# Optimization experiments

Measured on AMD Instinct MI355X. Metric: run time of the kernel, lower is better.

The kernel has to match this reference:

```python
import jax, jax.numpy as jnp
import numpy as np

BLOCK = 64      # block_size
NRAND = 3       # num_random_blocks
NUM_HEAD = 16
HEAD_DIM = 64
HIDDEN = 1024
PEN = -10000.0  # HF attn_mask_penalty


def _sparse_attn(q, k, v, band_mask, from_mask, to_mask, blocked_mask, rand_attn):
    # q,k,v: [B,H,S,D]; BigBird block-sparse attention (HF math).
    B, H, S, D = q.shape
    b, r = BLOCK, NRAND
    n = S // b
    rsd = 1.0 / (D ** 0.5)

    bq = q.reshape(B, H, n, b, D)
    bk = k.reshape(B, H, n, b, D)
    bv = v.reshape(B, H, n, b, D)

    bi = jnp.arange(B)[:, None, None, None]
    hi = jnp.arange(H)[None, :, None, None]
    # gathered random key/value blocks: [B,H,n-2,r*b,D]
    gk = bk[bi, hi, rand_attn].reshape(B, H, n - 2, r * b, D)
    gv = bv[bi, hi, rand_attn].reshape(B, H, n - 2, r * b, D)
    # random-block mask: [B,H,n-2,b,r*b]
    rm = blocked_mask[bi, rand_attn].reshape(B, H, n - 2, r * b)
    rand_mask = jnp.einsum("blq,bhlk->bhlqk", blocked_mask[:, 1:-1], rm)

    ones = lambda shp: jnp.ones(shp, q.dtype)

    # ---- first query block: attends to everything ----
    p = jnp.einsum("bhqd,bhkd->bhqk", bq[:, :, 0], k) * rsd + (1.0 - to_mask) * PEN
    c0 = jnp.einsum("bhqk,bhkd->bhqd", jax.nn.softmax(p, -1), v)[:, :, None]

    # ---- second query block: blocks 0,1,2,last + random ----
    k1 = jnp.concatenate([bk[:, :, 0], bk[:, :, 1], bk[:, :, 2], bk[:, :, -1], gk[:, :, 0]], axis=2)
    v1 = jnp.concatenate([bv[:, :, 0], bv[:, :, 1], bv[:, :, 2], bv[:, :, -1], gv[:, :, 0]], axis=2)
    p = jnp.einsum("bhqd,bhkd->bhqk", bq[:, :, 1], k1) * rsd
    seq_pad = jnp.concatenate([to_mask[..., :3 * b], to_mask[..., -b:], ones((B, 1, 1, r * b))], axis=3)
    rand_pad = jnp.concatenate([ones((B, H, b, 4 * b)), rand_mask[:, :, 0]], axis=3)
    p = p + (1.0 - jnp.minimum(seq_pad, rand_pad)) * PEN
    c1 = jnp.einsum("bhqk,bhkd->bhqd", jax.nn.softmax(p, -1), v1)[:, :, None]

    # ---- middle blocks 2..n-3: band(3 blocks) + first + last + random ----
    ek = jnp.concatenate([bk[:, :, 1:-3], bk[:, :, 2:-2], bk[:, :, 3:-1]], axis=3)  # [B,H,n-4,3b,D]
    ev = jnp.concatenate([bv[:, :, 1:-3], bv[:, :, 2:-2], bv[:, :, 3:-1]], axis=3)
    mq = bq[:, :, 2:-2]                                                              # [B,H,n-4,b,D]
    inner = jnp.einsum("bhlqd,bhlkd->bhlqk", mq, ek) * rsd + (1.0 - band_mask) * PEN
    randp = jnp.einsum("bhlqd,bhlkd->bhlqk", mq, gk[:, :, 1:-1]) * rsd + (1.0 - rand_mask[:, :, 1:-1]) * PEN
    firstp = jnp.einsum("bhlqd,bhkd->bhlqk", mq, bk[:, :, 0]) * rsd + (1.0 - to_mask[..., :b][:, :, None]) * PEN
    lastp = jnp.einsum("bhlqd,bhkd->bhlqk", mq, bk[:, :, -1]) * rsd + (1.0 - to_mask[..., -b:][:, :, None]) * PEN
    band = jnp.concatenate([firstp, inner, randp, lastp], axis=-1)  # [B,H,n-4,b,(5+r)*b]
    a = jax.nn.softmax(band, -1)
    cm = jnp.einsum("bhlqk,bhlkd->bhlqd", a[..., b:4 * b], ev)
    cm = cm + jnp.einsum("bhlqk,bhlkd->bhlqd", a[..., 4 * b:-b], gv[:, :, 1:-1])
    cm = cm + jnp.einsum("bhlqk,bhkd->bhlqd", a[..., :b], bv[:, :, 0])
    cm = cm + jnp.einsum("bhlqk,bhkd->bhlqd", a[..., -b:], bv[:, :, -1])

    # ---- second-last query block: blocks 0,-3,-2,-1 + random ----
    k2 = jnp.concatenate([bk[:, :, 0], bk[:, :, -3], bk[:, :, -2], bk[:, :, -1], gk[:, :, -1]], axis=2)
    v2 = jnp.concatenate([bv[:, :, 0], bv[:, :, -3], bv[:, :, -2], bv[:, :, -1], gv[:, :, -1]], axis=2)
    p = jnp.einsum("bhqd,bhkd->bhqk", bq[:, :, -2], k2) * rsd
    seq_pad = jnp.concatenate([to_mask[..., :b], to_mask[..., -3 * b:], ones((B, 1, 1, r * b))], axis=3)
    rand_pad = jnp.concatenate([ones((B, H, b, 4 * b)), rand_mask[:, :, -1]], axis=3)
    p = p + (1.0 - jnp.minimum(seq_pad, rand_pad)) * PEN
    c2 = jnp.einsum("bhqk,bhkd->bhqd", jax.nn.softmax(p, -1), v2)[:, :, None]

    # ---- last query block: attends to everything ----
    p = jnp.einsum("bhqd,bhkd->bhqk", bq[:, :, -1], k) * rsd + (1.0 - to_mask) * PEN
    c3 = jnp.einsum("bhqk,bhkd->bhqd", jax.nn.softmax(p, -1), v)[:, :, None]

    ctx = jnp.concatenate([c0, c1, cm, c2, c3], axis=2).reshape(B, H, S, D)
    ctx = ctx * from_mask  # [B,1,S,1]
    return ctx.transpose(0, 2, 1, 3).reshape(B, S, H * D)


def setup_inputs() -> dict:
    key = jax.random.key(0)
    ks = jax.random.split(key, 12)
    B, L = 2, 4064
    S = 4096
    n = S // BLOCK
    sc = 0.02
    inp = {
        "X": jax.random.normal(ks[0], (B, L, HIDDEN), jnp.float32),
        "Wq": jax.random.normal(ks[1], (HIDDEN, NUM_HEAD * HEAD_DIM), jnp.float32) * sc,
        "b_q": jnp.zeros((NUM_HEAD * HEAD_DIM,), jnp.float32),
        "Wk": jax.random.normal(ks[2], (HIDDEN, NUM_HEAD * HEAD_DIM), jnp.float32) * sc,
        "b_k": jnp.zeros((NUM_HEAD * HEAD_DIM,), jnp.float32),
        "Wv": jax.random.normal(ks[3], (HIDDEN, NUM_HEAD * HEAD_DIM), jnp.float32) * sc,
        "b_v": jnp.zeros((NUM_HEAD * HEAD_DIM,), jnp.float32),
        "Wo": jax.random.normal(ks[4], (NUM_HEAD * HEAD_DIM, HIDDEN), jnp.float32) * sc,
        "b_o": jnp.zeros((HIDDEN,), jnp.float32),
        "band_mask": jnp.ones((B, 1, n - 4, BLOCK, 3 * BLOCK), jnp.float32),
        "from_mask": jnp.ones((B, 1, S, 1), jnp.float32),
        "to_mask": jnp.ones((B, 1, 1, S), jnp.float32),
        "blocked_encoder_mask": jnp.ones((B, n, BLOCK), jnp.float32),
        "rand_attn": jax.random.randint(ks[5], (B, NUM_HEAD, n - 2, NRAND), 0, n, jnp.int32),
    }
    return inp


def reference(X, Wq, b_q, Wk, b_k, Wv, b_v, Wo, b_o,
              band_mask, from_mask, to_mask, blocked_encoder_mask, rand_attn):
    B, L, _ = X.shape
    pad = BLOCK - L % BLOCK  # matches torch wrapper (pads full block if L % b == 0)
    Xp = jnp.pad(X, ((0, 0), (0, pad), (0, 0)))
    S = L + pad

    def proj(W, bias):
        return (Xp @ W + bias).reshape(B, S, NUM_HEAD, HEAD_DIM).transpose(0, 2, 1, 3)

    q, k, v = proj(Wq, b_q), proj(Wk, b_k), proj(Wv, b_v)
    attn = _sparse_attn(q, k, v, band_mask, from_mask, to_mask, blocked_encoder_mask, rand_attn)
    out = attn @ Wo + b_o
    return out[:, :L]
```

## Files before the change

### kernel.cpp

```cpp
#include <hip/hip_runtime.h>

#define BB 2
#define SEQ 4096
#define LQ 4064
#define HID 1024
#define NH 16
#define HD 64
#define NB 64
#define BLK 64
#define NR 3
#define PENV -10000.0f

typedef __bf16 bf16;
typedef __bf16 bf16x8 __attribute__((ext_vector_type(8)));
typedef float floatx4 __attribute__((ext_vector_type(4)));

#define MEMFENCE asm volatile("" ::: "memory")

__device__ inline floatx4 mfma16(bf16x8 a, bf16x8 b, floatx4 c) {
    return __builtin_amdgcn_mfma_f32_16x16x32_bf16(a, b, c, 0, 0, 0);
}

__device__ inline void async_ld16(const bf16* g, bf16* l) {
    __builtin_amdgcn_global_load_lds(
        (const __attribute__((address_space(1))) unsigned int*)g,
        (__attribute__((address_space(3))) unsigned int*)l, 16, 0, 0);
}

__device__ inline void stage_k2(const bf16* kkbh, bf16* dst, int kb0, int kb1, int tid) {
    #pragma unroll
    for (int it = 0; it < 2; it++) {
        int o = (it * 256 + tid) * 16;
        int row = o >> 7;
        int c16 = (o >> 4) & 7;
        int srcel = row * 64 + ((c16 ^ (row & 7)) << 3);
        async_ld16(kkbh + (size_t)kb0 * (BLK * HD) + srcel, dst + (o >> 1));
        async_ld16(kkbh + (size_t)kb1 * (BLK * HD) + srcel, dst + 4096 + (o >> 1));
    }
}

__global__ __launch_bounds__(256) void cast_pad_x(const float* __restrict__ X,
                                                  bf16* __restrict__ Xp) {
    int t = blockIdx.x * 256 + threadIdx.x;
    int c4 = t & 255;
    int row = t >> 8;
    int b = row >> 12;
    int s = row & 4095;
    float4 v = make_float4(0.f, 0.f, 0.f, 0.f);
    if (s < LQ) {
        v = reinterpret_cast<const float4*>(X + ((size_t)(b * LQ + s)) * HID)[c4];
    }
    union { bf16 h[4]; uint2 u; } o;
    o.h[0] = (bf16)v.x; o.h[1] = (bf16)v.y; o.h[2] = (bf16)v.z; o.h[3] = (bf16)v.w;
    *reinterpret_cast<uint2*>(Xp + (size_t)row * HID + c4 * 4) = o.u;
}

__global__ __launch_bounds__(256) void transpose_w(const float* __restrict__ Wq,
                                                   const float* __restrict__ Wk,
                                                   const float* __restrict__ Wv,
                                                   const float* __restrict__ Wo,
                                                   bf16* __restrict__ WqkvT,
                                                   bf16* __restrict__ WoT) {
    __shared__ float tile[64][65];
    int sel = blockIdx.z;
    const float* src = (sel == 0) ? Wq : (sel == 1) ? Wk : (sel == 2) ? Wv : Wo;
    bf16* dst = (sel < 3) ? (WqkvT + (size_t)sel * HID * HID) : WoT;
    int j0 = blockIdx.x * 64, k0 = blockIdx.y * 64;
    int tx = threadIdx.x, ty = threadIdx.y;
    for (int i = 0; i < 16; i++) {
        int k = ty + i * 4;
        tile[k][tx] = src[(size_t)(k0 + k) * HID + j0 + tx];
    }
    __syncthreads();
    for (int i = 0; i < 16; i++) {
        int j = ty + i * 4;
        dst[(size_t)(j0 + j) * HID + k0 + tx] = (bf16)tile[tx][j];
    }
}

__global__ __launch_bounds__(256) void transpose_band(const float* __restrict__ band,
                                                      float* __restrict__ bandT) {
    __shared__ float tile[64][65];
    int kt = blockIdx.x;
    int lrow = blockIdx.y;
    int b = blockIdx.z;
    const float* src = band + ((size_t)(b * (NB - 4) + lrow) * BLK) * 192;
    float* dst = bandT + ((size_t)(b * (NB - 4) + lrow) * 192) * BLK;
    int tx = threadIdx.x, ty = threadIdx.y;
    for (int i = 0; i < 16; i++) {
        int qq = i * 4 + ty;
        tile[qq][tx] = src[(size_t)qq * 192 + kt * 64 + tx];
    }
    __syncthreads();
    for (int i = 0; i < 16; i++) {
        int k = i * 4 + ty;
        dst[(size_t)(kt * 64 + k) * BLK + tx] = tile[tx][k];
    }
}

__global__ __launch_bounds__(256) void mask_viol(const float* __restrict__ tom,
                                                 const float* __restrict__ blocked,
                                                 const float* __restrict__ band,
                                                 int* __restrict__ flags) {
    int which = blockIdx.y, b = blockIdx.z;
    const float* src;
    size_t n;
    if (which == 0)      { src = tom     + (size_t)b * SEQ;                  n = SEQ; }
    else if (which == 1) { src = blocked + (size_t)b * NB * BLK;             n = NB * BLK; }
    else                 { src = band    + (size_t)b * (NB - 4) * BLK * 192; n = (size_t)(NB - 4) * BLK * 192; }
    const float4* s4 = (const float4*)src;
    size_t n4 = n >> 2;
    int bad = 0;
    for (size_t i = blockIdx.x * 256 + threadIdx.x; i < n4; i += 240 * 256) {
        float4 v = s4[i];
        bad |= (v.x != 1.0f) | (v.y != 1.0f) | (v.z != 1.0f) | (v.w != 1.0f);
    }
    if (__any(bad) && (threadIdx.x & 63) == 0)
        atomicOr(&flags[which * BB + b], 1);
}

__global__ __launch_bounds__(256) void gemm_qkv(const bf16* __restrict__ Xp,
                                                const bf16* __restrict__ WT,
                                                const float* __restrict__ bq,
                                                const float* __restrict__ bk,
                                                const float* __restrict__ bv,
                                                bf16* __restrict__ qo,
                                                bf16* __restrict__ ko,
                                                bf16* __restrict__ vt) {
    __shared__ __align__(16) char smem[36864];
    bf16* As = (bf16*)smem;
    bf16* Bs = As + 128 * 64;
    int tid = threadIdx.x;
    int wave = tid >> 6, lane = tid & 63;
    int quad = lane >> 4, lm = lane & 15;
    int id = blockIdx.x;
    int xcd = id & 7, slot = id >> 3;
    int tile_m = (xcd * 8 + (slot & 7)) * 128;
    int tile_n = (slot >> 3) * 128;
    int wm = (wave & 1) * 64, wn = (wave >> 1) * 64;

    floatx4 acc[4][4] = {};

    for (int k0 = 0; k0 < HID; k0 += 64) {
        __syncthreads();
        for (int it = 0; it < 4; it++) {
            int c = it * 256 + tid;
            int row = c >> 3, col = (c & 7) * 8;
            async_ld16(Xp + (size_t)(tile_m + row) * HID + k0 + col, &As[c * 8]);
            async_ld16(WT + (size_t)(tile_n + row) * HID + k0 + col, &Bs[c * 8]);
        }
        __syncthreads();
        for (int ks = 0; ks < 64; ks += 32) {
            bf16x8 a[4], b[4];
            for (int i = 0; i < 4; i++)
                a[i] = *reinterpret_cast<const bf16x8*>(&As[(wm + i * 16 + lm) * 64 + ks + quad * 8]);
            for (int j = 0; j < 4; j++)
                b[j] = *reinterpret_cast<const bf16x8*>(&Bs[(wn + j * 16 + lm) * 64 + ks + quad * 8]);
            for (int i = 0; i < 4; i++)
                for (int j = 0; j < 4; j++)
                    acc[i][j] = mfma16(a[i], b[j], acc[i][j]);
        }
    }

    int which = tile_n >> 10;
    int hc_base = (tile_n + wn) & 1023;
    int h = hc_base >> 6;
    const float* bias = (which == 0) ? bq : (which == 1) ? bk : bv;
    __syncthreads();
    bf16* ep = (bf16*)smem + wave * (64 * 72);

    if (which < 2) {
        #pragma unroll
        for (int i = 0; i < 4; i++)
            #pragma unroll
            for (int j = 0; j < 4; j++) {
                float bsv = bias[hc_base + j * 16 + lm];
                #pragma unroll
                for (int r = 0; r < 4; r++) {
                    float val = acc[i][j][r] + bsv;
                    if (which == 0) val *= 0.125f;
                    ep[(i * 16 + quad * 4 + r) * 72 + j * 16 + lm] = (bf16)val;
                }
            }
        __builtin_amdgcn_wave_barrier();
        int s_glob = tile_m + wm + lane;
        int b_ = s_glob >> 12, s = s_glob & 4095;
        bf16* dstb = ((which == 0) ? qo : ko) + ((size_t)((b_ * NH + h) * SEQ + s)) * HD;
        #pragma unroll
        for (int c = 0; c < 8; c++)
            *reinterpret_cast<uint4*>(dstb + c * 8) =
                *reinterpret_cast<const uint4*>(ep + lane * 72 + c * 8);
    } else {
        #pragma unroll
        for (int i = 0; i < 4; i++)
            #pragma unroll
            for (int j = 0; j < 4; j++) {
                float bsv = bias[hc_base + j * 16 + lm];
                #pragma unroll
                for (int r = 0; r < 4; r++) {
                    float val = acc[i][j][r] + bsv;
                    ep[(j * 16 + lm) * 72 + i * 16 + quad * 4 + r] = (bf16)val;
                }
            }
        __builtin_amdgcn_wave_barrier();
        int s_base = tile_m + wm;
        int b_ = s_base >> 12, s0 = s_base & 4095;
        bf16* dstb = vt + ((size_t)((b_ * NH + h) * HD + lane)) * SEQ + s0;
        #pragma unroll
        for (int c = 0; c < 8; c++)
            *reinterpret_cast<uint4*>(dstb + c * 8) =
                *reinterpret_cast<const uint4*>(ep + lane * 72 + c * 8);
    }
}

__global__ __launch_bounds__(256, 2) void attn_kernel(const bf16* __restrict__ q,
                                                      const bf16* __restrict__ kk,
                                                      const bf16* __restrict__ vt,
                                                      const float* __restrict__ bandT,
                                                      const float* __restrict__ fromm,
                                                      const float* __restrict__ tom,
                                                      const float* __restrict__ blocked,
                                                      const int* __restrict__ rand_attn,
                                                      const int* __restrict__ flags,
                                                      bf16* __restrict__ attn) {
    __shared__ __align__(16) char smem[32768];
    bf16* sK = (bf16*)smem;

    int tid = threadIdx.x, wave = tid >> 6, lane = tid & 63;
    int quad = lane >> 4, lm = lane & 15;
    int sw = lm & 7;
    int bh = blockIdx.x;
    int b = bh >> 4, h = bh & 15;
    size_t bh_base = (size_t)bh * SEQ * HD;
    int x = blockIdx.y;
    bool fullmode = (x < 8);
    int l, sub;
    if (fullmode) { l = (x >> 2) ? (NB - 1) : 0; sub = x & 3; }
    else          { l = x - 7;                   sub = wave;  }

    bool do_to = flags[b] != 0;
    bool do_bl = flags[BB + b] != 0;
    bool do_bd = flags[2 * BB + b] != 0;

    unsigned long long kbp = 0ull;
    unsigned int typ_p = 0u;
    if (!fullmode) {
        int base;
        if (l == 1) {
            kbp = (1ull << 8) | (2ull << 16) | ((unsigned long long)(NB - 1) << 24);
            base = 4;
        } else if (l == NB - 2) {
            kbp = ((unsigned long long)(NB - 3) << 8) | ((unsigned long long)(NB - 2) << 16) |
                  ((unsigned long long)(NB - 1) << 24);
            base = 4;
        } else {
            kbp = ((unsigned long long)(l - 1) << 8) | ((unsigned long long)l << 16) |
                  ((unsigned long long)(l + 1) << 24) | ((unsigned long long)(NB - 1) << 32);
            typ_p = (1u << 4) | (2u << 8) | (3u << 12);
            base = 5;
        }
        const int* ra = rand_attn + ((size_t)(b * NH + h) * (NB - 2) + (l - 1)) * NR;
        #pragma unroll
        for (int r = 0; r < NR; r++) {
            int rv = __builtin_amdgcn_readfirstlane(ra[r]);
            kbp   |= (unsigned long long)(rv & 63) << ((base + r) * 8);
            typ_p |= 4u << ((base + r) * 4);
        }
        for (int i = base + NR; i < 8; i++) typ_p |= 5u << (i * 4);
    }

    bf16x8 aq0 = *reinterpret_cast<const bf16x8*>(
        q + bh_base + (size_t)(l * BLK + sub * 16 + lm) * HD + quad * 8);
    bf16x8 aq1 = *reinterpret_cast<const bf16x8*>(
        q + bh_base + (size_t)(l * BLK + sub * 16 + lm) * HD + 32 + quad * 8);
    float mq = blocked[((size_t)b * NB + l) * BLK + sub * 16 + lm];

    if (!fullmode) {
        MEMFENCE;
        int a0 = (int)((kbp >> 0) & 63),  a1 = (int)((kbp >> 8) & 63);
        int b0 = (int)((kbp >> 16) & 63), b1 = (int)((kbp >> 24) & 63);
        stage_k2(kk + bh_base, sK + 0,    a0, a1, tid);
        stage_k2(kk + bh_base, sK + 8192, b0, b1, tid);
        MEMFENCE;
    }

    floatx4 ctx[4] = {};
    float mrun = -1e30f, lrun = 0.f;

    int sbase = ((quad & 1) << 5) + lm;
    int fhi = quad >> 1;

    int nch = fullmode ? 8 : 4;
    for (int ch = 0; ch < nch; ch++) {
        int i0 = ch * 2, i1 = i0 + 1;
        int kb0, kb1, ty0, ty1;
        if (fullmode) {
            kb0 = __builtin_amdgcn_readfirstlane(wave * 16 + i0);
            kb1 = kb0 + 1;
            ty0 = 0; ty1 = 0;
        } else {
            kb0 = __builtin_amdgcn_readfirstlane((int)((kbp >> (i0 * 8)) & 63));
            kb1 = __builtin_amdgcn_readfirstlane((int)((kbp >> (i1 * 8)) & 63));
            ty0 = (int)((typ_p >> (i0 * 4)) & 15);
            ty1 = (int)((typ_p >> (i1 * 4)) & 15);
        }

        const bf16* v0p = vt + bh_base + (size_t)kb0 * BLK;
        bf16x8 vf0[4][2];
        #pragma unroll
        for (int dj = 0; dj < 4; dj++) {
            vf0[dj][0] = *reinterpret_cast<const bf16x8*>(v0p + (size_t)(dj * 16 + lm) * SEQ + quad * 8);
            vf0[dj][1] = *reinterpret_cast<const bf16x8*>(v0p + (size_t)(dj * 16 + lm) * SEQ + 32 + quad * 8);
        }
        MEMFENCE;

        floatx4 sc[2][4];
        if (!fullmode) {
            if (ch < 3) asm volatile("s_waitcnt vmcnt(8)" ::: "memory");
            else        asm volatile("s_waitcnt vmcnt(16)" ::: "memory");
            __builtin_amdgcn_s_barrier();
            const bf16* kbuf = sK + (ch & 1) * 8192;
            __builtin_amdgcn_s_setprio(1);
            #pragma unroll
            for (int u = 0; u < 2; u++) {
                bf16x8 ka[4], kb_[4];
                #pragma unroll
                for (int f = 0; f < 4; f++) {
                    int rowb = (f * 16 + lm) * 64;
                    ka[f]  = *reinterpret_cast<const bf16x8*>(
                        kbuf + u * 4096 + rowb + ((quad ^ sw) << 3));
                    kb_[f] = *reinterpret_cast<const bf16x8*>(
                        kbuf + u * 4096 + rowb + (((quad | 4) ^ sw) << 3));
                }
                #pragma unroll
                for (int f = 0; f < 4; f++) {
                    floatx4 z = {0.f, 0.f, 0.f, 0.f};
                    z = mfma16(ka[f], aq0, z);
                    z = mfma16(kb_[f], aq1, z);
                    sc[u][f] = z;
                }
            }
            __builtin_amdgcn_s_setprio(0);
        } else {
            const bf16* k0p = kk + bh_base + (size_t)kb0 * (BLK * HD);
            const bf16* k1p = kk + bh_base + (size_t)kb1 * (BLK * HD);
            bf16x8 kfa[2][4], kfb[2][4];
            #pragma unroll
            for (int f = 0; f < 4; f++) {
                kfa[0][f] = *reinterpret_cast<const bf16x8*>(k0p + (f * 16 + lm) * HD + quad * 8);
                kfb[0][f] = *reinterpret_cast<const bf16x8*>(k0p + (f * 16 + lm) * HD + 32 + quad * 8);
                kfa[1][f] = *reinterpret_cast<const bf16x8*>(k1p + (f * 16 + lm) * HD + quad * 8);
                kfb[1][f] = *reinterpret_cast<const bf16x8*>(k1p + (f * 16 + lm) * HD + 32 + quad * 8);
            }
            __builtin_amdgcn_s_setprio(1);
            #pragma unroll
            for (int u = 0; u < 2; u++)
                #pragma unroll
                for (int f = 0; f < 4; f++) {
                    floatx4 z = {0.f, 0.f, 0.f, 0.f};
                    z = mfma16(kfa[u][f], aq0, z);
                    z = mfma16(kfb[u][f], aq1, z);
                    sc[u][f] = z;
                }
            __builtin_amdgcn_s_setprio(0);
        }

        const bf16* v1p = vt + bh_base + (size_t)kb1 * BLK;
        bf16x8 vf1[4][2];
        #pragma unroll
        for (int dj = 0; dj < 4; dj++) {
            vf1[dj][0] = *reinterpret_cast<const bf16x8*>(v1p + (size_t)(dj * 16 + lm) * SEQ + quad * 8);
            vf1[dj][1] = *reinterpret_cast<const bf16x8*>(v1p + (size_t)(dj * 16 + lm) * SEQ + 32 + quad * 8);
        }
        MEMFENCE;

        {
            int kbs[2] = {kb0, kb1};
            int tys[2] = {ty0, ty1};
            #pragma unroll
            for (int u = 0; u < 2; u++) {
                int kb = kbs[u], typ = tys[u];
                if (typ == 0) {
                    if (do_to) {
                        #pragma unroll
                        for (int f = 0; f < 4; f++) {
                            float4 t4 = *reinterpret_cast<const float4*>(
                                tom + (size_t)b * SEQ + kb * BLK + f * 16 + quad * 4);
                            sc[u][f][0] += (1.f - t4.x) * PENV;
                            sc[u][f][1] += (1.f - t4.y) * PENV;
                            sc[u][f][2] += (1.f - t4.z) * PENV;
                            sc[u][f][3] += (1.f - t4.w) * PENV;
                        }
                    }
                } else if (typ == 4) {
                    if (do_bl) {
                        #pragma unroll
                        for (int f = 0; f < 4; f++) {
                            float4 t4 = *reinterpret_cast<const float4*>(
                                blocked + ((size_t)b * NB + kb) * BLK + f * 16 + quad * 4);
                            sc[u][f][0] += (1.f - mq * t4.x) * PENV;
                            sc[u][f][1] += (1.f - mq * t4.y) * PENV;
                            sc[u][f][2] += (1.f - mq * t4.z) * PENV;
                            sc[u][f][3] += (1.f - mq * t4.w) * PENV;
                        }
                    }
                } else if (typ != 5) {
                    if (do_bd) {
                        int t = typ - 1;
                        const float* bp = bandT + ((size_t)(b * (NB - 4) + (l - 2)) * 192 + t * 64) * BLK;
                        #pragma unroll
                        for (int f = 0; f < 4; f++)
                            #pragma unroll
                            for (int r = 0; r < 4; r++) {
                                float bm = bp[(size_t)(f * 16 + quad * 4 + r) * BLK + sub * 16 + lm];
                                sc[u][f][r] += (1.f - bm) * PENV;
                            }
                    }
                } else {
                    #pragma unroll
                    for (int f = 0; f < 4; f++)
                        #pragma unroll
                        for (int r = 0; r < 4; r++) sc[u][f][r] += PENV;
                }
            }
        }

        float mx = -1e30f;
        #pragma unroll
        for (int u = 0; u < 2; u++)
            #pragma unroll
            for (int f = 0; f < 4; f++)
                #pragma unroll
                for (int r = 0; r < 4; r++) mx = fmaxf(mx, sc[u][f][r]);
        float a16 = __shfl_xor(mx, 16, 64);
        float a32 = __shfl_xor(mx, 32, 64);
        float a48 = __shfl_xor(mx, 48, 64);
        mx = fmaxf(fmaxf(mx, a16), fmaxf(a32, a48));
        float mnew = fmaxf(mrun, mx);
        float scale = __expf(mrun - mnew);
        #pragma unroll
        for (int dj = 0; dj < 4; dj++) ctx[dj] *= scale;
        mrun = mnew;

        float rs = 0.f;
        uint2 pk[2][4];
        #pragma unroll
        for (int u = 0; u < 2; u++)
            #pragma unroll
            for (int f = 0; f < 4; f++) {
                float p0 = __expf(sc[u][f][0] - mnew);
                float p1 = __expf(sc[u][f][1] - mnew);
                float p2 = __expf(sc[u][f][2] - mnew);
                float p3 = __expf(sc[u][f][3] - mnew);
                rs += (p0 + p1) + (p2 + p3);
                union { bf16 hh[4]; uint2 u2; } pu;
                pu.hh[0] = (bf16)p0; pu.hh[1] = (bf16)p1;
                pu.hh[2] = (bf16)p2; pu.hh[3] = (bf16)p3;
                pk[u][f] = pu.u2;
            }
        lrun = lrun * scale + rs;

        bf16x8 pb[2][2];
        #pragma unroll
        for (int u = 0; u < 2; u++) {
            unsigned g0x[4], g0y[4], g1x[4], g1y[4];
            #pragma unroll
            for (int f = 0; f < 4; f++) {
                g0x[f] = (unsigned)__shfl((int)pk[u][f].x, sbase, 64);
                g0y[f] = (unsigned)__shfl((int)pk[u][f].y, sbase, 64);
                g1x[f] = (unsigned)__shfl((int)pk[u][f].x, sbase + 16, 64);
                g1y[f] = (unsigned)__shfl((int)pk[u][f].y, sbase + 16, 64);
            }
            union { unsigned v[4]; bf16x8 hv; } lo, hi;
            lo.v[0] = fhi ? g0x[1] : g0x[0];
            lo.v[1] = fhi ? g0y[1] : g0y[0];
            lo.v[2] = fhi ? g1x[1] : g1x[0];
            lo.v[3] = fhi ? g1y[1] : g1y[0];
            hi.v[0] = fhi ? g0x[3] : g0x[2];
            hi.v[1] = fhi ? g0y[3] : g0y[2];
            hi.v[2] = fhi ? g1x[3] : g1x[2];
            hi.v[3] = fhi ? g1y[3] : g1y[2];
            pb[u][0] = lo.hv;
            pb[u][1] = hi.hv;
        }

        if (!fullmode && ch >= 1 && ch + 1 < 4) {
            int na = __builtin_amdgcn_readfirstlane((int)((kbp >> ((ch + 1) * 16)) & 63));
            int nb = __builtin_amdgcn_readfirstlane((int)((kbp >> ((ch + 1) * 16 + 8)) & 63));
            stage_k2(kk + bh_base, sK + ((ch + 1) & 1) * 8192, na, nb, tid);
            MEMFENCE;
        }

        __builtin_amdgcn_s_setprio(1);
        #pragma unroll
        for (int dj = 0; dj < 4; dj++) {
            ctx[dj] = mfma16(vf0[dj][0], pb[0][0], ctx[dj]);
            ctx[dj] = mfma16(vf0[dj][1], pb[0][1], ctx[dj]);
        }
        #pragma unroll
        for (int dj = 0; dj < 4; dj++) {
            ctx[dj] = mfma16(vf1[dj][0], pb[1][0], ctx[dj]);
            ctx[dj] = mfma16(vf1[dj][1], pb[1][1], ctx[dj]);
        }
        __builtin_amdgcn_s_setprio(0);
    }

    {
        float b16 = __shfl_xor(lrun, 16, 64);
        float b32 = __shfl_xor(lrun, 32, 64);
        float b48 = __shfl_xor(lrun, 48, 64);
        lrun = (lrun + b16) + (b32 + b48);
    }

    if (!fullmode) {
        int sq = l * BLK + sub * 16 + lm;
        float w = (1.f / lrun) * fromm[(size_t)b * SEQ + sq];
        bf16* dst = attn + ((size_t)(b * SEQ + sq)) * HID + h * HD;
        #pragma unroll
        for (int dj = 0; dj < 4; dj++) {
            union { bf16 hh[4]; uint2 u2; } o;
            #pragma unroll
            for (int r = 0; r < 4; r++) o.hh[r] = (bf16)(ctx[dj][r] * w);
            *reinterpret_cast<uint2*>(dst + dj * 16 + quad * 4) = o.u2;
        }
    } else {
        float* ctxL = (float*)smem;
        float* mL   = (float*)(smem + 16384);
        float* lL   = (float*)(smem + 16640);
        __syncthreads();
        #pragma unroll
        for (int dj = 0; dj < 4; dj++)
            #pragma unroll
            for (int r = 0; r < 4; r++)
                ctxL[wave * 1024 + (dj * 16 + quad * 4 + r) * 16 + lm] = ctx[dj][r];
        if (quad == 0) { mL[wave * 16 + lm] = mrun; lL[wave * 16 + lm] = lrun; }
        __syncthreads();
        int qq = tid & 15, dbase = (tid >> 4) * 4;
        float M = -1e30f;
        for (int w = 0; w < 4; w++) M = fmaxf(M, mL[w * 16 + qq]);
        float e[4], Lt = 0.f;
        for (int w = 0; w < 4; w++) { e[w] = __expf(mL[w * 16 + qq] - M); Lt += lL[w * 16 + qq] * e[w]; }
        int sq = l * BLK + sub * 16 + qq;
        float wgt = (1.f / Lt) * fromm[(size_t)b * SEQ + sq];
        union { bf16 hh[4]; uint2 u2; } o;
        #pragma unroll
        for (int dd = 0; dd < 4; dd++) {
            float acc = 0.f;
            for (int w = 0; w < 4; w++) acc += ctxL[w * 1024 + (dbase + dd) * 16 + qq] * e[w];
            o.hh[dd] = (bf16)(acc * wgt);
        }
        *reinterpret_cast<uint2*>(attn + ((size_t)(b * SEQ + sq)) * HID + h * HD + dbase) = o.u2;
    }
}

__global__ __launch_bounds__(256) void gemm_out(const bf16* __restrict__ A,
                                                const bf16* __restrict__ WoT,
                                                const float* __restrict__ bo,
                                                float* __restrict__ out) {
    __shared__ __align__(16) char smem[65536];
    int tid = threadIdx.x;
    int wave = tid >> 6, lane = tid & 63;
    int quad = lane >> 4, lm = lane & 15;
    int id = blockIdx.x;
    int xcd = id & 7, slot = id >> 3;
    int tile_m = (xcd * 8 + (slot & 7)) * 128;
    int tile_n = (slot >> 3) * 128;
    int wm = (wave & 1) * 64, wn = (wave >> 1) * 64;

    floatx4 acc[4][4] = {};

    {
        bf16* base = (bf16*)smem;
        #pragma unroll
        for (int it = 0; it < 4; it++) {
            int c = it * 256 + tid;
            int row = c >> 3, col = (c & 7) * 8;
            async_ld16(A + (size_t)(tile_m + row) * HID + col, &base[c * 8]);
            async_ld16(WoT + (size_t)(tile_n + row) * HID + col, &base[8192 + c * 8]);
        }
    }
    __syncthreads();

    for (int t = 0; t < 16; t++) {
        if (t < 15) {
            bf16* base = (bf16*)smem + ((t + 1) & 1) * 16384;
            int k0 = (t + 1) * 64;
            #pragma unroll
            for (int it = 0; it < 4; it++) {
                int c = it * 256 + tid;
                int row = c >> 3, col = (c & 7) * 8;
                async_ld16(A + (size_t)(tile_m + row) * HID + k0 + col, &base[c * 8]);
                async_ld16(WoT + (size_t)(tile_n + row) * HID + k0 + col, &base[8192 + c * 8]);
            }
        }
        const bf16* As = (const bf16*)smem + (t & 1) * 16384;
        const bf16* Bs = As + 8192;
        #pragma unroll
        for (int ks = 0; ks < 64; ks += 32) {
            bf16x8 a[4], b[4];
            for (int i = 0; i < 4; i++)
                a[i] = *reinterpret_cast<const bf16x8*>(&As[(wm + i * 16 + lm) * 64 + ks + quad * 8]);
            for (int j = 0; j < 4; j++)
                b[j] = *reinterpret_cast<const bf16x8*>(&Bs[(wn + j * 16 + lm) * 64 + ks + quad * 8]);
            for (int i = 0; i < 4; i++)
                for (int j = 0; j < 4; j++)
                    acc[i][j] = mfma16(a[i], b[j], acc[i][j]);
        }
        __syncthreads();
    }

    for (int i = 0; i < 4; i++) {
        for (int j = 0; j < 4; j++) {
            int nn = tile_n + wn + j * 16 + lm;
            float bsv = bo[nn];
            for (int r = 0; r < 4; r++) {
                int mm = tile_m + wm + i * 16 + quad * 4 + r;
                int b_ = mm >> 12, s = mm & 4095;
                if (s < LQ)
                    out[((size_t)(b_ * LQ + s)) * HID + nn] = acc[i][j][r] + bsv;
            }
        }
    }
}

extern "C" void kernel_launch(void* const* d_in, const int* in_sizes, int n_in,
                              void* d_out, int out_size, void* d_ws, size_t ws_size,
                              hipStream_t stream) {
    const float* X       = (const float*)d_in[0];
    const float* Wq      = (const float*)d_in[1];
    const float* bq      = (const float*)d_in[2];
    const float* Wk      = (const float*)d_in[3];
    const float* bk      = (const float*)d_in[4];
    const float* Wv      = (const float*)d_in[5];
    const float* bv      = (const float*)d_in[6];
    const float* Wo      = (const float*)d_in[7];
    const float* bo      = (const float*)d_in[8];
    const float* band    = (const float*)d_in[9];
    const float* fromm   = (const float*)d_in[10];
    const float* tom     = (const float*)d_in[11];
    const float* blocked = (const float*)d_in[12];
    const int*   randa   = (const int*)d_in[13];
    float* out = (float*)d_out;

    char* ws = (char*)d_ws;
    bf16* Xp    = (bf16*)(ws + 0);
    bf16* WqkvT = (bf16*)(ws + 16777216);
    bf16* WoT   = (bf16*)(ws + 23068672);
    bf16* qb    = (bf16*)(ws + 25165824);
    bf16* kb    = (bf16*)(ws + 41943040);
    bf16* vtb   = (bf16*)(ws + 58720256);
    bf16* attnb = Xp;
    float* bandT = (float*)WqkvT;
    int* flagsp = (int*)(ws + 16777216 + 5898240);

    cast_pad_x<<<dim3(8192), dim3(256), 0, stream>>>(X, Xp);
    transpose_w<<<dim3(16, 16, 4), dim3(64, 4), 0, stream>>>(Wq, Wk, Wv, Wo, WqkvT, WoT);
    gemm_qkv<<<dim3(1536), dim3(256), 0, stream>>>(Xp, WqkvT, bq, bk, bv, qb, kb, vtb);
    transpose_band<<<dim3(3, NB - 4, BB), dim3(64, 4), 0, stream>>>(band, bandT);
    hipMemsetAsync(flagsp, 0, 3 * BB * sizeof(int), stream);
    mask_viol<<<dim3(240, 3, BB), dim3(256), 0, stream>>>(tom, blocked, band, flagsp);
    attn_kernel<<<dim3(BB * NH, 70), dim3(256), 0, stream>>>(qb, kb, vtb, bandT, fromm, tom,
                                                             blocked, randa, flagsp, attnb);
    gemm_out<<<dim3(512), dim3(256), 0, stream>>>(attnb, WoT, bo, out);
}
```

Measured before the change: 334.1 us.

## Double-buffer QKV GEMM LDS tiles and drop setprio hints in attention

Rewrites the QKV projection GEMM main loop to use two LDS buffers, prefetching the next K-slice with async global-to-LDS loads while MFMAs run on the current slice. Each iteration now needs one barrier instead of two. Shared memory grows from 36 KB to 64 KB, which may lower occupancy. Separately removes the s_setprio boosts around MFMA sections in the attention kernel.

```diff
diff --git a/kernel.cpp b/kernel.cpp
--- a/kernel.cpp
+++ b/kernel.cpp
@@ -127,9 +127,7 @@
                                                 bf16* __restrict__ qo,
                                                 bf16* __restrict__ ko,
                                                 bf16* __restrict__ vt) {
-    __shared__ __align__(16) char smem[36864];
-    bf16* As = (bf16*)smem;
-    bf16* Bs = As + 128 * 64;
+    __shared__ __align__(16) char smem[65536];
     int tid = threadIdx.x;
     int wave = tid >> 6, lane = tid & 63;
     int quad = lane >> 4, lm = lane & 15;
@@ -141,15 +139,33 @@
 
     floatx4 acc[4][4] = {};
 
-    for (int k0 = 0; k0 < HID; k0 += 64) {
-        __syncthreads();
+    {
+        bf16* base = (bf16*)smem;
+        #pragma unroll
         for (int it = 0; it < 4; it++) {
             int c = it * 256 + tid;
             int row = c >> 3, col = (c & 7) * 8;
-            async_ld16(Xp + (size_t)(tile_m + row) * HID + k0 + col, &As[c * 8]);
-            async_ld16(WT + (size_t)(tile_n + row) * HID + k0 + col, &Bs[c * 8]);
-        }
-        __syncthreads();
+            async_ld16(Xp + (size_t)(tile_m + row) * HID + col, &base[c * 8]);
+            async_ld16(WT + (size_t)(tile_n + row) * HID + col, &base[8192 + c * 8]);
+        }
+    }
+    __syncthreads();
+
+    for (int t = 0; t < 16; t++) {
+        if (t < 15) {
+            bf16* base = (bf16*)smem + ((t + 1) & 1) * 16384;
+            int k0 = (t + 1) * 64;
+            #pragma unroll
+            for (int it = 0; it < 4; it++) {
+                int c = it * 256 + tid;
+                int row = c >> 3, col = (c & 7) * 8;
+                async_ld16(Xp + (size_t)(tile_m + row) * HID + k0 + col, &base[c * 8]);
+                async_ld16(WT + (size_t)(tile_n + row) * HID + k0 + col, &base[8192 + c * 8]);
+            }
+        }
+        const bf16* As = (const bf16*)smem + (t & 1) * 16384;
+        const bf16* Bs = As + 8192;
+        #pragma unroll
         for (int ks = 0; ks < 64; ks += 32) {
             bf16x8 a[4], b[4];
             for (int i = 0; i < 4; i++)
@@ -160,13 +176,13 @@
                 for (int j = 0; j < 4; j++)
                     acc[i][j] = mfma16(a[i], b[j], acc[i][j]);
         }
+        __syncthreads();
     }
 
     int which = tile_n >> 10;
     int hc_base = (tile_n + wn) & 1023;
     int h = hc_base >> 6;
     const float* bias = (which == 0) ? bq : (which == 1) ? bk : bv;
-    __syncthreads();
     bf16* ep = (bf16*)smem + wave * (64 * 72);
 
     if (which < 2) {
@@ -320,7 +336,6 @@
             else        asm volatile("s_waitcnt vmcnt(16)" ::: "memory");
             __builtin_amdgcn_s_barrier();
             const bf16* kbuf = sK + (ch & 1) * 8192;
-            __builtin_amdgcn_s_setprio(1);
             #pragma unroll
             for (int u = 0; u < 2; u++) {
                 bf16x8 ka[4], kb_[4];
@@ -340,7 +355,6 @@
                     sc[u][f] = z;
                 }
             }
-            __builtin_amdgcn_s_setprio(0);
         } else {
             const bf16* k0p = kk + bh_base + (size_t)kb0 * (BLK * HD);
             const bf16* k1p = kk + bh_base + (size_t)kb1 * (BLK * HD);
@@ -352,7 +366,6 @@
                 kfa[1][f] = *reinterpret_cast<const bf16x8*>(k1p + (f * 16 + lm) * HD + quad * 8);
                 kfb[1][f] = *reinterpret_cast<const bf16x8*>(k1p + (f * 16 + lm) * HD + 32 + quad * 8);
             }
-            __builtin_amdgcn_s_setprio(1);
             #pragma unroll
             for (int u = 0; u < 2; u++)
                 #pragma unroll
@@ -362,7 +375,6 @@
                     z = mfma16(kfb[u][f], aq1, z);
                     sc[u][f] = z;
                 }
-            __builtin_amdgcn_s_setprio(0);
         }
 
         const bf16* v1p = vt + bh_base + (size_t)kb1 * BLK;
@@ -491,7 +503,6 @@
             MEMFENCE;
         }
 
-        __builtin_amdgcn_s_setprio(1);
         #pragma unroll
         for (int dj = 0; dj < 4; dj++) {
             ctx[dj] = mfma16(vf0[dj][0], pb[0][0], ctx[dj]);
@@ -502,7 +513,6 @@
             ctx[dj] = mfma16(vf1[dj][0], pb[1][0], ctx[dj]);
             ctx[dj] = mfma16(vf1[dj][1], pb[1][1], ctx[dj]);
         }
-        __builtin_amdgcn_s_setprio(0);
     }
 
     {
```

Result: no change. 329.3 us, median of 2 (-1.4%).
